# Optimization experiments

Measured on AMD Instinct MI355X. Metric: run time of the kernel, lower is better.

The kernel has to match this reference:

```python
import jax, jax.numpy as jnp
import numpy as np
from jax import lax

H = 1024
NH = 16
R = 32
B, S = 32, 1024
LN_EPS = 1e-5

def _gelu(x):
    return jax.nn.gelu(x, approximate=False)

def setup_inputs() -> dict:
    key = jax.random.key(0)
    ks = jax.random.split(key, 24)
    w = lambda k, shape: jax.random.normal(k, shape, jnp.float32) * 0.02
    d = {}
    d['computation_results'] = jax.random.normal(ks[0], (B, S, H), jnp.float32)
    d['max_steps'] = 16
    # rule selector: Linear(H,H), GELU, Linear(H,R)
    d['rule_w1'] = w(ks[1], (H, H)); d['rule_b1'] = jnp.zeros((H,))
    d['rule_w2'] = w(ks[2], (R, H)); d['rule_b2'] = jnp.zeros((R,))
    d['rule_emb'] = jax.random.normal(ks[3], (R, H), jnp.float32)
    # MultiheadAttention packed in-proj [3H,H] and out-proj [H,H]
    d['attn_in_w'] = w(ks[4], (3 * H, H)); d['attn_in_b'] = jnp.zeros((3 * H,))
    d['attn_out_w'] = w(ks[5], (H, H)); d['attn_out_b'] = jnp.zeros((H,))
    # 2-layer LSTM, PyTorch gate order i,f,g,o
    d['lstm_wih0'] = w(ks[6], (4 * H, H)); d['lstm_whh0'] = w(ks[7], (4 * H, H))
    d['lstm_bih0'] = jnp.zeros((4 * H,)); d['lstm_bhh0'] = jnp.zeros((4 * H,))
    d['lstm_wih1'] = w(ks[8], (4 * H, H)); d['lstm_whh1'] = w(ks[9], (4 * H, H))
    d['lstm_bih1'] = jnp.zeros((4 * H,)); d['lstm_bhh1'] = jnp.zeros((4 * H,))
    # step generator: Linear(H,2H), LayerNorm(2H), GELU, Linear(2H,H)
    d['gen_w1'] = w(ks[10], (2 * H, H)); d['gen_b1'] = jnp.zeros((2 * H,))
    d['gen_ln_g'] = jnp.ones((2 * H,)); d['gen_ln_b'] = jnp.zeros((2 * H,))
    d['gen_w2'] = w(ks[11], (H, 2 * H)); d['gen_b2'] = jnp.zeros((H,))
    # step validator: Linear(2H,H), GELU, Linear(H,1), Sigmoid
    d['val_w1'] = w(ks[12], (H, 2 * H)); d['val_b1'] = jnp.zeros((H,))
    d['val_w2'] = w(ks[13], (1, H)); d['val_b2'] = jnp.zeros((1,))
    # proof verifier: Linear(H,H), GELU, Linear(H,1), Sigmoid
    d['ver_w1'] = w(ks[14], (H, H)); d['ver_b1'] = jnp.zeros((H,))
    d['ver_w2'] = w(ks[15], (1, H)); d['ver_b2'] = jnp.zeros((1,))
    return d


def reference(computation_results, max_steps, rule_w1, rule_b1, rule_w2, rule_b2, rule_emb,
              attn_in_w, attn_in_b, attn_out_w, attn_out_b,
              lstm_wih0, lstm_whh0, lstm_bih0, lstm_bhh0,
              lstm_wih1, lstm_whh1, lstm_bih1, lstm_bhh1,
              gen_w1, gen_b1, gen_ln_g, gen_ln_b, gen_w2, gen_b2,
              val_w1, val_b1, val_w2, val_b2,
              ver_w1, ver_b1, ver_w2, ver_b2):
    comp = computation_results
    b, s, h = comp.shape
    dh = h // NH
    scale = dh ** -0.5
    wq, wk, wv = jnp.split(attn_in_w, 3, axis=0)
    bq, bk, bv = jnp.split(attn_in_b, 3, axis=0)
    # K/V projections of the static context, computed once outside the step loop
    K = (comp @ wk.T + bk).reshape(b, s, NH, dh)  # [B,S,NH,dh]
    V = (comp @ wv.T + bv).reshape(b, s, NH, dh)
    lstm_params = ((lstm_wih0, lstm_whh0, lstm_bih0, lstm_bhh0),
                   (lstm_wih1, lstm_whh1, lstm_bih1, lstm_bhh1))

    def step(carry, _):
        ps, hmem, cmem = carry  # ps: [B,H]; hmem/cmem: [2,B,H]
        # rule selection
        logits = _gelu(ps @ rule_w1.T + rule_b1) @ rule_w2.T + rule_b2
        probs = jax.nn.softmax(logits, axis=-1)  # [B,R]
        sel = probs @ rule_emb  # [B,H]
        # single-query multi-head attention over computation context
        q = (ps @ wq.T + bq).reshape(b, NH, dh) * scale
        scores = jnp.einsum('bhd,bshd->bhs', q, K)
        a = jax.nn.softmax(scores, axis=-1)  # [B,NH,S]
        ctx = jnp.einsum('bhs,bshd->bhd', a, V).reshape(b, h) @ attn_out_w.T + attn_out_b
        attn_avg = a.mean(axis=1)  # head-averaged weights, [B,S]
        # 2-layer LSTM cell, one timestep
        x = ps
        hs, cs = [], []
        for l, (wih, whh, bih, bhh) in enumerate(lstm_params):
            g = x @ wih.T + bih + hmem[l] @ whh.T + bhh
            gi, gf, gg, go = jnp.split(g, 4, axis=-1)
            cn = jax.nn.sigmoid(gf) * cmem[l] + jax.nn.sigmoid(gi) * jnp.tanh(gg)
            hn = jax.nn.sigmoid(go) * jnp.tanh(cn)
            hs.append(hn); cs.append(cn); x = hn
        mem_out = x
        # step generator with LayerNorm+GELU
        si = ps + sel + ctx + mem_out
        z = si @ gen_w1.T + gen_b1
        mu = z.mean(axis=-1, keepdims=True)
        var = ((z - mu) ** 2).mean(axis=-1, keepdims=True)
        z = (z - mu) / jnp.sqrt(var + LN_EPS) * gen_ln_g + gen_ln_b
        nxt = _gelu(z) @ gen_w2.T + gen_b2
        val = jax.nn.sigmoid(_gelu(jnp.concatenate([ps, nxt], axis=-1) @ val_w1.T + val_b1) @ val_w2.T + val_b2)
        return (nxt, jnp.stack(hs), jnp.stack(cs)), (nxt, probs, val, attn_avg)

    init_state = comp[:, 0, :]
    carry0 = (init_state, jnp.zeros((2, b, h), comp.dtype), jnp.zeros((2, b, h), comp.dtype))
    (final, _, _), (steps, probs, vals, attn) = lax.scan(step, carry0, None, length=int(max_steps))
    proof_steps = jnp.concatenate([init_state[None], steps], axis=0)  # [T+1,B,H]
    proof_validity = jax.nn.sigmoid(_gelu(final @ ver_w1.T + ver_b1) @ ver_w2.T + ver_b2)  # [B,1]
    return proof_steps, proof_validity, probs, vals, attn
```

## Files before the change

### kernel.cpp

```cpp
#include <hip/hip_runtime.h>

typedef unsigned short u16;
typedef unsigned int u32;
typedef __attribute__((ext_vector_type(8))) short short8v;
typedef __attribute__((ext_vector_type(4))) float f32x4;

#define MFMA16(a,b,c) __builtin_amdgcn_mfma_f32_16x16x32_bf16((a),(b),(c),0,0,0)

__device__ __forceinline__ u16 f2bf(float f){
  u32 u = __float_as_uint(f);
  return (u16)((u + 0x7fffu + ((u >> 16) & 1u)) >> 16);
}
__device__ __forceinline__ float bf2f(u16 h){ return __uint_as_float(((u32)h) << 16); }
__device__ __forceinline__ float gelu_f(float x){ return 0.5f * x * (1.f + erff(x * 0.70710678118654752f)); }
__device__ __forceinline__ float sigm_f(float x){ return 1.f / (1.f + __expf(-x)); }
__device__ __forceinline__ void acc4(float4& a, const float4 b){ a.x+=b.x; a.y+=b.y; a.z+=b.z; a.w+=b.w; }

__device__ __forceinline__ void gl16(const void* g, void* l){
  __builtin_amdgcn_global_load_lds((const __attribute__((address_space(1))) u32*)g,
                                   (__attribute__((address_space(3))) u32*)l, 16, 0, 0);
}

struct CastJobs { const float* s[13]; u16* d[13]; int start[14]; };
__global__ __launch_bounds__(256) void cast_all_k(CastJobs J){
  int bx = blockIdx.x, j = 0;
  #pragma unroll
  for (int t = 0; t < 13; t++) if (bx >= J.start[t + 1]) j = t + 1;
  int i = (bx - J.start[j]) * 1024 + threadIdx.x * 4;
  float4 v = *(const float4*)(J.s[j] + i);
  ushort4 o; o.x = f2bf(v.x); o.y = f2bf(v.y); o.z = f2bf(v.z); o.w = f2bf(v.w);
  *(ushort4*)(J.d[j] + i) = o;
}

__global__ __launch_bounds__(256) void cast_k(const float* __restrict__ s, u16* __restrict__ d, int n){
  int i = (blockIdx.x * 256 + threadIdx.x) * 4;
  if (i + 3 < n){
    float4 v = *(const float4*)(s + i);
    ushort4 o; o.x = f2bf(v.x); o.y = f2bf(v.y); o.z = f2bf(v.z); o.w = f2bf(v.w);
    *(ushort4*)(d + i) = o;
  }
}

__global__ __launch_bounds__(256) void init_k(const float* __restrict__ comp, float* ps0, float* outp,
                                              float* h0, float* c0, float* h1, float* c1){
  int i = blockIdx.x * 256 + threadIdx.x;
  int b = i >> 10, hh = i & 1023;
  float v = comp[(size_t)b * 1048576 + hh];
  ps0[i] = v; outp[i] = v;
  h0[i] = 0.f; c0[i] = 0.f; h1[i] = 0.f; c1[i] = 0.f;
}

__global__ __launch_bounds__(256) void gemmkv_k(const u16* __restrict__ compb,
    const u16* __restrict__ Wk, const u16* __restrict__ Wv,
    const float* __restrict__ bk, const float* __restrict__ bv,
    u16* __restrict__ Kt, u16* __restrict__ Vb)
{
  __shared__ u16 As[128 * 64];
  __shared__ u16 Bs[128 * 64];
  int tid = threadIdx.x;
  int x = blockIdx.x;
  int xcd = x & 7, p = x >> 3;
  int cpanel = xcd * 32 + (p >> 3);
  int wpanel = p & 7;
  int isK = (blockIdx.z != 0);
  const u16 *msrc, *nsrc; int m0, n0;
  if (!isK){ m0 = cpanel * 128; n0 = wpanel * 128; msrc = compb; nsrc = Wv; }
  else     { m0 = wpanel * 128; n0 = cpanel * 128; msrc = Wk;    nsrc = compb; }

  int w = tid >> 6, l = tid & 63, lr = l & 15, lk = l >> 4;
  int wm = (w >> 1) * 64, wn = (w & 1) * 64;
  f32x4 acc[4][4];
  #pragma unroll
  for (int i = 0; i < 4; i++)
    #pragma unroll
    for (int j = 0; j < 4; j++) acc[i][j] = (f32x4){0.f,0.f,0.f,0.f};

  for (int kc = 0; kc < 1024; kc += 64){
    #pragma unroll
    for (int r = 0; r < 4; r++){
      int s = tid + r * 256;
      int row = s >> 3, pp = s & 7;
      int lg = pp ^ (row & 7);
      gl16(msrc + (size_t)(m0 + row) * 1024 + kc + lg * 8, As + s * 8);
      gl16(nsrc + (size_t)(n0 + row) * 1024 + kc + lg * 8, Bs + s * 8);
    }
    __syncthreads();
    #pragma unroll
    for (int kk = 0; kk < 2; kk++){
      short8v a[4], bb[4];
      #pragma unroll
      for (int mi = 0; mi < 4; mi++){
        int row = wm + mi * 16 + lr;
        int ph = (kk * 4 + lk) ^ (row & 7);
        a[mi] = *(const short8v*)(As + row * 64 + ph * 8);
      }
      #pragma unroll
      for (int ni = 0; ni < 4; ni++){
        int row = wn + ni * 16 + lr;
        int ph = (kk * 4 + lk) ^ (row & 7);
        bb[ni] = *(const short8v*)(Bs + row * 64 + ph * 8);
      }
      #pragma unroll
      for (int mi = 0; mi < 4; mi++)
        #pragma unroll
        for (int ni = 0; ni < 4; ni++)
          acc[mi][ni] = MFMA16(a[mi], bb[ni], acc[mi][ni]);
    }
    __syncthreads();
  }
  #pragma unroll
  for (int mi = 0; mi < 4; mi++)
    #pragma unroll
    for (int ni = 0; ni < 4; ni++)
      #pragma unroll
      for (int r = 0; r < 4; r++){
        int row = m0 + wm + mi * 16 + lk * 4 + r;
        int col = n0 + wn + ni * 16 + lr;
        if (!isK){
          Vb[(size_t)row * 1024 + col] = f2bf(acc[mi][ni][r] + bv[col]);
        } else {
          int b = col >> 10, s = col & 1023;
          Kt[((size_t)b * 1024 + row) * 1024 + s] = f2bf(acc[mi][ni][r] + bk[row]);
        }
      }
}

struct LinSeg {
  const float* X0; const float* Xa; const float* Xb; const float* Xc;
  const u16* W1; const float* b1;
  const float* Y; const u16* W2; const float* b2;
  float* out; float* out2;
  int K1, ld1, K2, ld2, N, act, gate;
  float scale;
  float* stats;
  const float* lng; const float* lnb; const float* lnstats;
  const float* cprev; float* cout; float* hout;
};

__device__ __forceinline__ short8v pack8(float4 v0, float4 v1){
  short8v r;
  r[0]=(short)f2bf(v0.x); r[1]=(short)f2bf(v0.y); r[2]=(short)f2bf(v0.z); r[3]=(short)f2bf(v0.w);
  r[4]=(short)f2bf(v1.x); r[5]=(short)f2bf(v1.y); r[6]=(short)f2bf(v1.z); r[7]=(short)f2bf(v1.w);
  return r;
}

__device__ __forceinline__ short8v load_sum8(const LinSeg& S, int row, int kb){
  size_t o = (size_t)row * S.K1 + kb;
  float4 v0 = *(const float4*)(S.X0 + o);
  float4 v1 = *(const float4*)(S.X0 + o + 4);
  if (S.lng){
    float mu = S.lnstats[row] * (1.f / 2048.f);
    float ms = S.lnstats[32 + row] * (1.f / 2048.f);
    float rstd = rsqrtf(ms - mu * mu + 1e-5f);
    float4 g0 = *(const float4*)(S.lng + kb), g1 = *(const float4*)(S.lng + kb + 4);
    float4 b0 = *(const float4*)(S.lnb + kb), b1 = *(const float4*)(S.lnb + kb + 4);
    v0.x = gelu_f((v0.x - mu) * rstd * g0.x + b0.x);
    v0.y = gelu_f((v0.y - mu) * rstd * g0.y + b0.y);
    v0.z = gelu_f((v0.z - mu) * rstd * g0.z + b0.z);
    v0.w = gelu_f((v0.w - mu) * rstd * g0.w + b0.w);
    v1.x = gelu_f((v1.x - mu) * rstd * g1.x + b1.x);
    v1.y = gelu_f((v1.y - mu) * rstd * g1.y + b1.y);
    v1.z = gelu_f((v1.z - mu) * rstd * g1.z + b1.z);
    v1.w = gelu_f((v1.w - mu) * rstd * g1.w + b1.w);
  } else {
    if (S.Xa){ acc4(v0, *(const float4*)(S.Xa + o)); acc4(v1, *(const float4*)(S.Xa + o + 4)); }
    if (S.Xb){ acc4(v0, *(const float4*)(S.Xb + o)); acc4(v1, *(const float4*)(S.Xb + o + 4)); }
    if (S.Xc){ acc4(v0, *(const float4*)(S.Xc + o)); acc4(v1, *(const float4*)(S.Xc + o + 4)); }
  }
  return pack8(v0, v1);
}
__device__ __forceinline__ short8v load_y8(const float* __restrict__ p){
  return pack8(*(const float4*)(p), *(const float4*)(p + 4));
}

typedef float Red32[32][32];

__device__ void lin_body(const LinSeg& S, int bi, int tid, Red32* red){
  int c0 = bi * 32, j0 = bi * 8;
  int w = tid >> 6, l = tid & 63, lr = l & 15, lk = l >> 4;
  int wc0 = S.gate ? ((lr >> 3) << 10) + j0 + (lr & 7) : c0 + lr;
  int wc1 = S.gate ? (((lr + 16) >> 3) << 10) + j0 + ((lr + 16) & 7) : c0 + lr + 16;
  f32x4 acc[2][2];
  #pragma unroll
  for (int i = 0; i < 2; i++)
    #pragma unroll
    for (int j = 0; j < 2; j++) acc[i][j] = (f32x4){0.f,0.f,0.f,0.f};

  {
    int chunk = S.K1 >> 3;
    int kb0 = w * chunk + lk * 8;
    for (int kk = 0; kk < chunk; kk += 32){
      int kb = kb0 + kk;
      short8v a0 = load_sum8(S, lr, kb);
      short8v a1 = load_sum8(S, lr + 16, kb);
      short8v w0 = *(const short8v*)(S.W1 + (size_t)wc0 * S.ld1 + kb);
      short8v w1 = *(const short8v*)(S.W1 + (size_t)wc1 * S.ld1 + kb);
      acc[0][0] = MFMA16(a0, w0, acc[0][0]);
      acc[0][1] = MFMA16(a0, w1, acc[0][1]);
      acc[1][0] = MFMA16(a1, w0, acc[1][0]);
      acc[1][1] = MFMA16(a1, w1, acc[1][1]);
    }
  }
  if (S.Y){
    int chunk = S.K2 >> 3;
    int kb0 = w * chunk + lk * 8;
    for (int kk = 0; kk < chunk; kk += 32){
      int kb = kb0 + kk;
      short8v a0 = load_y8(S.Y + (size_t)lr * S.K2 + kb);
      short8v a1 = load_y8(S.Y + (size_t)(lr + 16) * S.K2 + kb);
      short8v w0 = *(const short8v*)(S.W2 + (size_t)wc0 * S.ld2 + kb);
      short8v w1 = *(const short8v*)(S.W2 + (size_t)wc1 * S.ld2 + kb);
      acc[0][0] = MFMA16(a0, w0, acc[0][0]);
      acc[0][1] = MFMA16(a0, w1, acc[0][1]);
      acc[1][0] = MFMA16(a1, w0, acc[1][0]);
      acc[1][1] = MFMA16(a1, w1, acc[1][1]);
    }
  }
  #pragma unroll
  for (int mi = 0; mi < 2; mi++)
    #pragma unroll
    for (int ni = 0; ni < 2; ni++)
      #pragma unroll
      for (int r = 0; r < 4; r++)
        red[w][mi * 16 + lk * 4 + r][ni * 16 + lr] = acc[mi][ni][r];
  __syncthreads();
  if (S.gate){
    if (tid < 256){
      int row = tid >> 3, j = tid & 7;
      float s[4];
      #pragma unroll
      for (int g = 0; g < 4; g++){
        float v = 0.f;
        #pragma unroll
        for (int ww = 0; ww < 8; ww++) v += red[ww][row][g * 8 + j];
        s[g] = v;
      }
      int gc = j0 + j;
      float gI = s[0] + S.b1[gc]        + S.b2[gc];
      float gF = s[1] + S.b1[1024 + gc] + S.b2[1024 + gc];
      float gG = s[2] + S.b1[2048 + gc] + S.b2[2048 + gc];
      float gO = s[3] + S.b1[3072 + gc] + S.b2[3072 + gc];
      int idx = row * 1024 + gc;
      float cN = sigm_f(gF) * S.cprev[idx] + sigm_f(gI) * tanhf(gG);
      S.cout[idx] = cN;
      S.hout[idx] = sigm_f(gO) * tanhf(cN);
    }
    return;
  }
  float vout[2]; int iout[2];
  int cnt = 0;
  for (int i = tid; i < 1024; i += 512){
    int row = i >> 5, col = i & 31;
    float v = 0.f;
    #pragma unroll
    for (int ww = 0; ww < 8; ww++) v += red[ww][row][col];
    v += S.b1[c0 + col];
    if (S.b2) v += S.b2[c0 + col];
    if (S.act == 1) v = gelu_f(v);
    else if (S.act == 2) v *= S.scale;
    S.out[(size_t)row * S.N + c0 + col] = v;
    if (S.out2) S.out2[(size_t)row * S.N + c0 + col] = v;
    vout[cnt] = v; iout[cnt] = i; cnt++;
  }
  if (S.stats){
    __syncthreads();
    float* rf = (float*)red;
    rf[iout[0]] = vout[0]; rf[1024 + iout[0]] = vout[0] * vout[0];
    rf[iout[1]] = vout[1]; rf[1024 + iout[1]] = vout[1] * vout[1];
    __syncthreads();
    if (tid < 32){
      float s = 0.f, s2 = 0.f;
      #pragma unroll
      for (int cc = 0; cc < 32; cc++){ s += rf[tid * 32 + cc]; s2 += rf[1024 + tid * 32 + cc]; }
      atomicAdd(S.stats + tid, s);
      atomicAdd(S.stats + 32 + tid, s2);
    }
  }
}

__global__ __launch_bounds__(512) void linmulti_k(LinSeg s0, LinSeg s1, LinSeg s2, int n0, int n1,
                                                  float* zero64){
  __shared__ float red[8][32][32];
  int bx = blockIdx.x, tid = threadIdx.x;
  if (zero64 && bx == 0 && tid < 64) zero64[tid] = 0.f;
  if (bx < n0) lin_body(s0, bx, tid, red);
  else if (bx < n0 + n1) lin_body(s1, bx - n0, tid, red);
  else lin_body(s2, bx - n0 - n1, tid, red);
}

__global__ __launch_bounds__(512) void valver_k(const u16* __restrict__ vw1, const float* __restrict__ vb1,
    const u16* __restrict__ verw1, const float* __restrict__ verb1,
    const float* __restrict__ proof, float* __restrict__ v1){
  __shared__ float red[8][32][32];
  int t = blockIdx.y;
  LinSeg S = {};
  if (t < 16){
    S.X0 = proof + (size_t)t * 32768; S.K1 = 1024; S.W1 = vw1; S.ld1 = 2048; S.b1 = vb1;
    S.Y = proof + (size_t)(t + 1) * 32768; S.K2 = 1024; S.W2 = vw1 + 1024; S.ld2 = 2048;
  } else {
    S.X0 = proof + (size_t)16 * 32768; S.K1 = 1024; S.W1 = verw1; S.ld1 = 1024; S.b1 = verb1;
  }
  S.out = v1 + (size_t)t * 32768; S.N = 1024; S.act = 1;
  lin_body(S, blockIdx.x, threadIdx.x, red);
}

__global__ __launch_bounds__(256) void dotsig_b_k(const float* __restrict__ v1,
    const float* __restrict__ w2v, const float* __restrict__ b2v,
    const float* __restrict__ w2ver, const float* __restrict__ b2ver,
    float* __restrict__ out_vals, float* __restrict__ out_valid){
  int t = blockIdx.x;
  const float* w = (t < 16) ? w2v : w2ver;
  const float* bs = (t < 16) ? b2v : b2ver;
  const float* x = v1 + (size_t)t * 32768;
  int b = threadIdx.x >> 3, l8 = threadIdx.x & 7;
  const float* xr = x + (size_t)b * 1024;
  float acc = 0.f;
  #pragma unroll 8
  for (int kk = 0; kk < 32; kk++){
    int k = kk * 32 + l8 * 4;
    float4 xv = *(const float4*)(xr + k);
    float4 wv = *(const float4*)(w + k);
    acc += xv.x * wv.x + xv.y * wv.y + xv.z * wv.z + xv.w * wv.w;
  }
  acc += __shfl_xor(acc, 1); acc += __shfl_xor(acc, 2); acc += __shfl_xor(acc, 4);
  if (l8 == 0){
    float r = sigm_f(acc + bs[0]);
    if (t < 16) out_vals[t * 32 + b] = r; else out_valid[b] = r;
  }
}

__global__ __launch_bounds__(256) void attn_r2_k(const float* __restrict__ q,
    const u16* __restrict__ Kt, const u16* __restrict__ Vb,
    float* __restrict__ afull, float* __restrict__ ctx0,
    const float* __restrict__ h1a, const float* __restrict__ w2, const float* __restrict__ b2,
    const float* __restrict__ emb, float* __restrict__ probs_out, float* __restrict__ sel)
{
  int tid = threadIdx.x;
  if (blockIdx.x >= 512){
    int b = blockIdx.x - 512;
    __shared__ float lg[32], pshared[32];
    int j = tid >> 3, l8 = tid & 7;
    const float* xr = h1a + b * 1024;
    const float* wr = w2 + j * 1024;
    float acc = 0.f;
    #pragma unroll 8
    for (int kk = 0; kk < 32; kk++){
      int k = kk * 32 + l8 * 4;
      float4 xv = *(const float4*)(xr + k);
      float4 wv = *(const float4*)(wr + k);
      acc += xv.x * wv.x + xv.y * wv.y + xv.z * wv.z + xv.w * wv.w;
    }
    acc += __shfl_xor(acc, 1); acc += __shfl_xor(acc, 2); acc += __shfl_xor(acc, 4);
    if (l8 == 0) lg[j] = acc + b2[j];
    __syncthreads();
    if (tid < 32){
      float v = lg[tid];
      float m = v;
      for (int o = 1; o < 32; o <<= 1) m = fmaxf(m, __shfl_xor(m, o));
      float e = __expf(v - m);
      float s = e;
      for (int o = 1; o < 32; o <<= 1) s += __shfl_xor(s, o);
      float p = e / s;
      pshared[tid] = p;
      probs_out[b * 32 + tid] = p;
    }
    __syncthreads();
    for (int j2 = tid; j2 < 1024; j2 += 256){
      float a2 = 0.f;
      #pragma unroll
      for (int r = 0; r < 32; r++) a2 += pshared[r] * emb[r * 1024 + j2];
      sel[b * 1024 + j2] = a2;
    }
    return;
  }
  int bh = blockIdx.x;
  int b = bh >> 4, h = bh & 15;
  __shared__ float qs[64];
  __shared__ float sc[1024];
  __shared__ float rmx[4], rsm[4];
  __shared__ float ctxp[8][64];
  if (tid < 64) qs[tid] = q[bh * 64 + tid];
  __syncthreads();
  const u32* kt = (const u32*)(Kt + (size_t)bh * 65536);
  float a0 = 0.f, a1 = 0.f, a2 = 0.f, a3 = 0.f;
  #pragma unroll 8
  for (int d = 0; d < 64; d++){
    float qd = qs[d];
    u32 p0 = kt[d * 512 + tid];
    u32 p1 = kt[d * 512 + tid + 256];
    a0 += qd * bf2f((u16)(p0 & 0xffff)); a1 += qd * bf2f((u16)(p0 >> 16));
    a2 += qd * bf2f((u16)(p1 & 0xffff)); a3 += qd * bf2f((u16)(p1 >> 16));
  }
  float mx = fmaxf(fmaxf(a0, a1), fmaxf(a2, a3));
  for (int o = 1; o < 64; o <<= 1) mx = fmaxf(mx, __shfl_xor(mx, o));
  if ((tid & 63) == 0) rmx[tid >> 6] = mx;
  __syncthreads();
  mx = fmaxf(fmaxf(rmx[0], rmx[1]), fmaxf(rmx[2], rmx[3]));
  float e0 = __expf(a0 - mx), e1 = __expf(a1 - mx), e2 = __expf(a2 - mx), e3 = __expf(a3 - mx);
  float sm = e0 + e1 + e2 + e3;
  for (int o = 1; o < 64; o <<= 1) sm += __shfl_xor(sm, o);
  if ((tid & 63) == 0) rsm[tid >> 6] = sm;
  __syncthreads();
  sm = rsm[0] + rsm[1] + rsm[2] + rsm[3];
  float inv = 1.f / sm;
  float* ar = afull + (size_t)bh * 1024;
  float2 w0 = make_float2(e0 * inv, e1 * inv);
  float2 w1 = make_float2(e2 * inv, e3 * inv);
  *(float2*)(sc + 2 * tid) = w0;       *(float2*)(ar + 2 * tid) = w0;
  *(float2*)(sc + 512 + 2 * tid) = w1; *(float2*)(ar + 512 + 2 * tid) = w1;
  __syncthreads();
  int d2 = (tid & 31) * 2, chunk = tid >> 5;
  const u16* vb = Vb + ((size_t)(b * 1024) * 16 + h) * 64 + d2;
  float c0 = 0.f, c1 = 0.f;
  for (int s = chunk * 128; s < chunk * 128 + 128; s++){
    u32 vv = *(const u32*)(vb + (size_t)s * 1024);
    float wv = sc[s];
    c0 += wv * bf2f((u16)(vv & 0xffff));
    c1 += wv * bf2f((u16)(vv >> 16));
  }
  *(float2*)&ctxp[chunk][d2] = make_float2(c0, c1);
  __syncthreads();
  if (tid < 64){
    float r = 0.f;
    #pragma unroll
    for (int c = 0; c < 8; c++) r += ctxp[c][tid];
    ctx0[bh * 64 + tid] = r;
  }
}

__global__ __launch_bounds__(256) void attnavg_all_k(const float* __restrict__ afull, float* __restrict__ out){
  int idx = blockIdx.x * 256 + threadIdx.x;
  int t = idx >> 15, r = idx & 32767;
  int b = r >> 10, s = r & 1023;
  const float* base = afull + (size_t)t * 524288 + (size_t)b * 16384;
  float acc = 0.f;
  #pragma unroll
  for (int h = 0; h < 16; h++) acc += base[h * 1024 + s];
  out[idx] = acc * (1.f / 16.f);
}

extern "C" void kernel_launch(void* const* d_in, const int* in_sizes, int n_in,
                              void* d_out, int out_size, void* d_ws, size_t ws_size,
                              hipStream_t stream) {
  const float* comp      = (const float*)d_in[0];
  const float* rule_w1   = (const float*)d_in[2];
  const float* rule_b1   = (const float*)d_in[3];
  const float* rule_w2   = (const float*)d_in[4];
  const float* rule_b2   = (const float*)d_in[5];
  const float* rule_emb  = (const float*)d_in[6];
  const float* attn_in_w = (const float*)d_in[7];
  const float* attn_in_b = (const float*)d_in[8];
  const float* attn_out_w= (const float*)d_in[9];
  const float* attn_out_b= (const float*)d_in[10];
  const float* wih0 = (const float*)d_in[11];
  const float* whh0 = (const float*)d_in[12];
  const float* bih0 = (const float*)d_in[13];
  const float* bhh0 = (const float*)d_in[14];
  const float* wih1 = (const float*)d_in[15];
  const float* whh1 = (const float*)d_in[16];
  const float* bih1 = (const float*)d_in[17];
  const float* bhh1 = (const float*)d_in[18];
  const float* gen_w1 = (const float*)d_in[19];
  const float* gen_b1 = (const float*)d_in[20];
  const float* ln_g   = (const float*)d_in[21];
  const float* ln_b   = (const float*)d_in[22];
  const float* gen_w2 = (const float*)d_in[23];
  const float* gen_b2 = (const float*)d_in[24];
  const float* val_w1 = (const float*)d_in[25];
  const float* val_b1 = (const float*)d_in[26];
  const float* val_w2 = (const float*)d_in[27];
  const float* val_b2 = (const float*)d_in[28];
  const float* ver_w1 = (const float*)d_in[29];
  const float* ver_b1 = (const float*)d_in[30];
  const float* ver_w2 = (const float*)d_in[31];
  const float* ver_b2 = (const float*)d_in[32];

  float* out_f     = (float*)d_out;
  float* out_proof = out_f;
  float* out_valid = out_f + 17 * 32768;
  float* out_probs = out_valid + 32;
  float* out_vals  = out_probs + 16 * 1024;
  float* out_attn  = out_vals + 16 * 32;

  char* wp = (char*)d_ws;
  auto carve = [&](size_t bytes) -> void* {
    void* p = (void*)wp; wp += (bytes + 255) & ~(size_t)255; return p;
  };
  u16* Kt    = (u16*)carve((size_t)33554432 * 2);
  u16* Vb    = (u16*)carve((size_t)33554432 * 2);
  u16* compb = (u16*)carve((size_t)33554432 * 2);
  float* afull_all = (float*)compb;
  u16* rw1b  = (u16*)carve(2097152);
  u16* wqb   = (u16*)carve(2097152);
  u16* wkb   = (u16*)carve(2097152);
  u16* wvb   = (u16*)carve(2097152);
  u16* aowb  = (u16*)carve(2097152);
  u16* wih0b = (u16*)carve(8388608);
  u16* whh0b = (u16*)carve(8388608);
  u16* wih1b = (u16*)carve(8388608);
  u16* whh1b = (u16*)carve(8388608);
  u16* gw1b  = (u16*)carve(4194304);
  u16* gw2b  = (u16*)carve(4194304);
  u16* vw1b  = (u16*)carve(4194304);
  u16* verw1b= (u16*)carve(2097152);
  float* psb[2]  = { (float*)carve(131072), (float*)carve(131072) };
  float* h0b[2]  = { (float*)carve(131072), (float*)carve(131072) };
  float* c0b[2]  = { (float*)carve(131072), (float*)carve(131072) };
  float* h1b[2]  = { (float*)carve(131072), (float*)carve(131072) };
  float* c1b[2]  = { (float*)carve(131072), (float*)carve(131072) };
  float* h1act = (float*)carve(131072);
  float* sel   = (float*)carve(131072);
  float* qbuf  = (float*)carve(131072);
  float* ctx0  = (float*)carve(131072);
  float* ctxb  = (float*)carve(131072);
  float* zbuf  = (float*)carve(262144);
  float* v1buf = (float*)carve(2228224);
  float* lnstats = (float*)carve(256);
  (void)ws_size; (void)in_sizes; (void)n_in; (void)out_size;

  CastJobs J;
  const float* srcs[13] = { rule_w1, attn_in_w, attn_in_w + 1048576, attn_in_w + 2097152,
                            attn_out_w, wih0, whh0, wih1, whh1, gen_w1, gen_w2, val_w1, ver_w1 };
  u16* dsts[13] = { rw1b, wqb, wkb, wvb, aowb, wih0b, whh0b, wih1b, whh1b, gw1b, gw2b, vw1b, verw1b };
  int sizes[13] = { 1048576, 1048576, 1048576, 1048576, 1048576,
                    4194304, 4194304, 4194304, 4194304, 2097152, 2097152, 2097152, 1048576 };
  int st = 0;
  for (int i = 0; i < 13; i++){ J.s[i] = srcs[i]; J.d[i] = dsts[i]; J.start[i] = st; st += sizes[i] / 1024; }
  J.start[13] = st;
  cast_all_k<<<dim3(st), dim3(256), 0, stream>>>(J);
  cast_k<<<dim3(32768), dim3(256), 0, stream>>>(comp, compb, 33554432);

  gemmkv_k<<<dim3(2048, 1, 2), dim3(256), 0, stream>>>(compb, wkb, wvb,
      attn_in_b + 1024, attn_in_b + 2048, Kt, Vb);

  init_k<<<dim3(128), dim3(256), 0, stream>>>(comp, psb[0], out_proof,
      h0b[0], c0b[0], h1b[0], c1b[0]);

  auto mkseg = [&](const float* X0, const float* Xa, const float* Xb, const float* Xc,
                   int K1, const u16* W1, int ld1, const float* bb1,
                   const float* Y, int K2, const u16* W2, int ld2, const float* bb2,
                   float* out, int N, int act, float scl, float* out2) -> LinSeg {
    LinSeg S = {};
    S.X0 = X0; S.Xa = Xa; S.Xb = Xb; S.Xc = Xc; S.K1 = K1; S.W1 = W1; S.ld1 = ld1; S.b1 = bb1;
    S.Y = Y; S.K2 = K2; S.W2 = W2; S.ld2 = ld2; S.b2 = bb2;
    S.out = out; S.N = N; S.act = act; S.scale = scl; S.out2 = out2;
    return S;
  };
  auto lin1 = [&](LinSeg S){
    linmulti_k<<<dim3(S.N / 32), dim3(512), 0, stream>>>(S, S, S, S.N / 32, 0, nullptr);
  };

  for (int t = 0; t < 16; t++){
    int cur = t & 1, nx = cur ^ 1;
    float* ps = psb[cur];
    float* afull_t = afull_all + (size_t)t * 524288;
    LinSeg sRule = mkseg(ps, 0, 0, 0, 1024, rw1b, 1024, rule_b1, 0, 0, 0, 0, 0, h1act, 1024, 1, 0.f, 0);
    LinSeg sQ    = mkseg(ps, 0, 0, 0, 1024, wqb, 1024, attn_in_b, 0, 0, 0, 0, 0, qbuf, 1024, 2, 0.125f, 0);
    LinSeg sL0   = mkseg(ps, 0, 0, 0, 1024, wih0b, 1024, bih0, h0b[cur], 1024, whh0b, 1024, bhh0,
                         0, 4096, 0, 0.f, 0);
    sL0.gate = 1; sL0.cprev = c0b[cur]; sL0.cout = c0b[nx]; sL0.hout = h0b[nx];
    linmulti_k<<<dim3(192), dim3(512), 0, stream>>>(sRule, sQ, sL0, 32, 32, nullptr);
    attn_r2_k<<<dim3(544), dim3(256), 0, stream>>>(qbuf, Kt, Vb, afull_t, ctx0,
        h1act, rule_w2, rule_b2, rule_emb, out_probs + t * 1024, sel);
    LinSeg sCtx = mkseg(ctx0, 0, 0, 0, 1024, aowb, 1024, attn_out_b, 0, 0, 0, 0, 0, ctxb, 1024, 0, 0.f, 0);
    LinSeg sL1  = mkseg(h0b[nx], 0, 0, 0, 1024, wih1b, 1024, bih1, h1b[cur], 1024, whh1b, 1024, bhh1,
                        0, 4096, 0, 0.f, 0);
    sL1.gate = 1; sL1.cprev = c1b[cur]; sL1.cout = c1b[nx]; sL1.hout = h1b[nx];
    linmulti_k<<<dim3(160), dim3(512), 0, stream>>>(sCtx, sL1, sL1, 32, 128, lnstats);
    LinSeg sG1 = mkseg(ps, sel, ctxb, h1b[nx], 1024, gw1b, 1024, gen_b1, 0, 0, 0, 0, 0,
                       zbuf, 2048, 0, 0.f, 0);
    sG1.stats = lnstats;
    lin1(sG1);
    LinSeg sG2 = mkseg(zbuf, 0, 0, 0, 2048, gw2b, 2048, gen_b2, 0, 0, 0, 0, 0,
                       psb[nx], 1024, 0, 0.f, out_proof + (size_t)(t + 1) * 32768);
    sG2.lng = ln_g; sG2.lnb = ln_b; sG2.lnstats = lnstats;
    lin1(sG2);
  }
  valver_k<<<dim3(32, 17), dim3(512), 0, stream>>>(vw1b, val_b1, verw1b, ver_b1, out_proof, v1buf);
  dotsig_b_k<<<dim3(17), dim3(256), 0, stream>>>(v1buf, val_w2, val_b2, ver_w2, ver_b2,
      out_vals, out_valid);
  attnavg_all_k<<<dim3(2048), dim3(256), 0, stream>>>(afull_all, out_attn);
}
```

Before: 1.925 ms.

## Fuse the 16-step recurrent loop into one persistent kernel with grid barriers

After: 7.126 ms. 3.7x slower.

```diff
diff --git a/kernel.cpp b/kernel.cpp
--- a/kernel.cpp
+++ b/kernel.cpp
@@ -19,6 +19,18 @@
 __device__ __forceinline__ void gl16(const void* g, void* l){
   __builtin_amdgcn_global_load_lds((const __attribute__((address_space(1))) u32*)g,
                                    (__attribute__((address_space(3))) u32*)l, 16, 0, 0);
+}
+
+__device__ __forceinline__ void gbar(unsigned* cnt, unsigned target){
+  __syncthreads();
+  if (threadIdx.x == 0){
+    __threadfence();
+    __hip_atomic_fetch_add(cnt, 1u, __ATOMIC_RELEASE, __HIP_MEMORY_SCOPE_AGENT);
+    while (__hip_atomic_load(cnt, __ATOMIC_ACQUIRE, __HIP_MEMORY_SCOPE_AGENT) < target)
+      __builtin_amdgcn_s_sleep(1);
+    __threadfence();
+  }
+  __syncthreads();
 }
 
 struct CastJobs { const float* s[13]; u16* d[13]; int start[14]; };
@@ -42,7 +54,9 @@
 }
 
 __global__ __launch_bounds__(256) void init_k(const float* __restrict__ comp, float* ps0, float* outp,
-                                              float* h0, float* c0, float* h1, float* c1){
+                                              float* h0, float* c0, float* h1, float* c1,
+                                              unsigned* barcnt){
+  if (blockIdx.x == 0 && threadIdx.x == 0) *barcnt = 0u;
   int i = blockIdx.x * 256 + threadIdx.x;
   int b = i >> 10, hh = i & 1023;
   float v = comp[(size_t)b * 1048576 + hh];
@@ -169,7 +183,7 @@
   }
   return pack8(v0, v1);
 }
-__device__ __forceinline__ short8v load_y8(const float* __restrict__ p){
+__device__ __forceinline__ short8v load_y8(const float* p){
   return pack8(*(const float4*)(p), *(const float4*)(p + 4));
 }
 
@@ -278,14 +292,186 @@
   }
 }
 
-__global__ __launch_bounds__(512) void linmulti_k(LinSeg s0, LinSeg s1, LinSeg s2, int n0, int n1,
-                                                  float* zero64){
+__device__ void attn_job(int bh, int tid, const float* q, const u16* Kt, const u16* Vb,
+                         float* afull, float* ctx0, float* shf){
+  float* qs = shf;
+  float* sc = shf + 64;
+  float* rr = shf + 1088;
+  float* ctxp = shf + 1104;
+  int b = bh >> 4, h = bh & 15;
+  if (tid < 64) qs[tid] = q[bh * 64 + tid];
+  __syncthreads();
+  const u32* kt = (const u32*)(Kt + (size_t)bh * 65536);
+  float a0 = 0.f, a1 = 0.f;
+  #pragma unroll 8
+  for (int d = 0; d < 64; d++){
+    float qd = qs[d];
+    u32 p0 = kt[d * 512 + tid];
+    a0 += qd * bf2f((u16)(p0 & 0xffff));
+    a1 += qd * bf2f((u16)(p0 >> 16));
+  }
+  float mx = fmaxf(a0, a1);
+  for (int o = 1; o < 64; o <<= 1) mx = fmaxf(mx, __shfl_xor(mx, o));
+  if ((tid & 63) == 0) rr[tid >> 6] = mx;
+  __syncthreads();
+  mx = rr[0];
+  #pragma unroll
+  for (int i = 1; i < 8; i++) mx = fmaxf(mx, rr[i]);
+  float e0 = __expf(a0 - mx), e1 = __expf(a1 - mx);
+  float sm = e0 + e1;
+  for (int o = 1; o < 64; o <<= 1) sm += __shfl_xor(sm, o);
+  if ((tid & 63) == 0) rr[8 + (tid >> 6)] = sm;
+  __syncthreads();
+  sm = 0.f;
+  #pragma unroll
+  for (int i = 0; i < 8; i++) sm += rr[8 + i];
+  float inv = 1.f / sm;
+  float2 wv = make_float2(e0 * inv, e1 * inv);
+  *(float2*)(sc + 2 * tid) = wv;
+  *(float2*)(afull + (size_t)bh * 1024 + 2 * tid) = wv;
+  __syncthreads();
+  int d2 = (tid & 31) * 2, chunk = tid >> 5;
+  const u16* vb = Vb + (size_t)(b * 1024 + chunk * 64) * 1024 + h * 64 + d2;
+  const float* scp = sc + chunk * 64;
+  float c0 = 0.f, c1 = 0.f;
+  for (int s = 0; s < 64; s++){
+    u32 vv = *(const u32*)(vb + (size_t)s * 1024);
+    float w = scp[s];
+    c0 += w * bf2f((u16)(vv & 0xffff));
+    c1 += w * bf2f((u16)(vv >> 16));
+  }
+  *(float2*)(ctxp + chunk * 64 + d2) = make_float2(c0, c1);
+  __syncthreads();
+  if (tid < 64){
+    float r = 0.f;
+    #pragma unroll
+    for (int c = 0; c < 16; c++) r += ctxp[c * 64 + tid];
+    ctx0[bh * 64 + tid] = r;
+  }
+}
+
+__device__ void rule2_job(int b, int tid, const float* h1a, const float* w2, const float* b2,
+                          const float* emb, float* probs_out, float* sel, float* shf){
+  float* lg = shf;
+  float* psh = shf + 32;
+  int j = tid >> 4, l16 = tid & 15;
+  const float* xr = h1a + b * 1024;
+  const float* wr = w2 + j * 1024;
+  float acc = 0.f;
+  #pragma unroll 4
+  for (int kk = 0; kk < 16; kk++){
+    int k = kk * 64 + l16 * 4;
+    float4 xv = *(const float4*)(xr + k);
+    float4 wv = *(const float4*)(wr + k);
+    acc += xv.x * wv.x + xv.y * wv.y + xv.z * wv.z + xv.w * wv.w;
+  }
+  acc += __shfl_xor(acc, 1); acc += __shfl_xor(acc, 2);
+  acc += __shfl_xor(acc, 4); acc += __shfl_xor(acc, 8);
+  if (l16 == 0) lg[j] = acc + b2[j];
+  __syncthreads();
+  if (tid < 32){
+    float v = lg[tid];
+    float m = v;
+    for (int o = 1; o < 32; o <<= 1) m = fmaxf(m, __shfl_xor(m, o));
+    float e = __expf(v - m);
+    float s = e;
+    for (int o = 1; o < 32; o <<= 1) s += __shfl_xor(s, o);
+    float p = e / s;
+    psh[tid] = p;
+    probs_out[b * 32 + tid] = p;
+  }
+  __syncthreads();
+  for (int j2 = tid; j2 < 1024; j2 += 512){
+    float a2 = 0.f;
+    #pragma unroll
+    for (int r = 0; r < 32; r++) a2 += psh[r] * emb[r * 1024 + j2];
+    sel[b * 1024 + j2] = a2;
+  }
+}
+
+struct StepParams {
+  const u16 *rw1b, *wqb, *wih0b, *whh0b, *aowb, *wih1b, *whh1b, *gw1b, *gw2b;
+  const float *rule_b1, *attn_in_b, *bih0, *bhh0, *rule_w2, *rule_b2, *rule_emb;
+  const float *attn_out_b, *bih1, *bhh1, *gen_b1, *gen_b2, *ln_g, *ln_b;
+  const u16 *Kt, *Vb;
+  float *ps0, *ps1, *h0a, *h0bb, *c0a, *c0bb, *h1aa, *h1bb, *c1a, *c1bb;
+  float *h1act, *sel, *qbuf, *ctx0, *ctxb, *zbuf, *lnstats;
+  float *afull_all, *out_probs, *out_proof;
+  unsigned* barcnt;
+};
+
+__global__ __launch_bounds__(512) void steploop_k(StepParams P){
   __shared__ float red[8][32][32];
+  float* shf = &red[0][0][0];
   int bx = blockIdx.x, tid = threadIdx.x;
-  if (zero64 && bx == 0 && tid < 64) zero64[tid] = 0.f;
-  if (bx < n0) lin_body(s0, bx, tid, red);
-  else if (bx < n0 + n1) lin_body(s1, bx - n0, tid, red);
-  else lin_body(s2, bx - n0 - n1, tid, red);
+  unsigned tgt = 0;
+  for (int t = 0; t < 16; t++){
+    float *ps, *psn, *h0c, *h0n, *c0c, *c0n, *h1c, *h1n, *c1c, *c1n;
+    if ((t & 1) == 0){
+      ps = P.ps0;  psn = P.ps1;
+      h0c = P.h0a; h0n = P.h0bb; c0c = P.c0a; c0n = P.c0bb;
+      h1c = P.h1aa; h1n = P.h1bb; c1c = P.c1a; c1n = P.c1bb;
+    } else {
+      ps = P.ps1;  psn = P.ps0;
+      h0c = P.h0bb; h0n = P.h0a; c0c = P.c0bb; c0n = P.c0a;
+      h1c = P.h1bb; h1n = P.h1aa; c1c = P.c1bb; c1n = P.c1a;
+    }
+    float* afull_t = P.afull_all + (size_t)t * 524288;
+
+    if (bx < 32){
+      LinSeg S = {}; S.X0 = ps; S.K1 = 1024; S.W1 = P.rw1b; S.ld1 = 1024; S.b1 = P.rule_b1;
+      S.out = P.h1act; S.N = 1024; S.act = 1;
+      lin_body(S, bx, tid, red);
+    } else if (bx < 64){
+      LinSeg S = {}; S.X0 = ps; S.K1 = 1024; S.W1 = P.wqb; S.ld1 = 1024; S.b1 = P.attn_in_b;
+      S.out = P.qbuf; S.N = 1024; S.act = 2; S.scale = 0.125f;
+      lin_body(S, bx - 32, tid, red);
+    } else if (bx < 192){
+      LinSeg S = {}; S.X0 = ps; S.K1 = 1024; S.W1 = P.wih0b; S.ld1 = 1024; S.b1 = P.bih0;
+      S.Y = h0c; S.K2 = 1024; S.W2 = P.whh0b; S.ld2 = 1024; S.b2 = P.bhh0;
+      S.gate = 1; S.cprev = c0c; S.cout = c0n; S.hout = h0n;
+      lin_body(S, bx - 64, tid, red);
+    }
+    gbar(P.barcnt, tgt += 256);
+
+    for (int j = bx; j < 544; j += 256){
+      if (j < 512) attn_job(j, tid, P.qbuf, P.Kt, P.Vb, afull_t, P.ctx0, shf);
+      else rule2_job(j - 512, tid, P.h1act, P.rule_w2, P.rule_b2, P.rule_emb,
+                     P.out_probs + t * 1024, P.sel, shf);
+      __syncthreads();
+    }
+    gbar(P.barcnt, tgt += 256);
+
+    if (bx < 32){
+      LinSeg S = {}; S.X0 = P.ctx0; S.K1 = 1024; S.W1 = P.aowb; S.ld1 = 1024; S.b1 = P.attn_out_b;
+      S.out = P.ctxb; S.N = 1024;
+      lin_body(S, bx, tid, red);
+    } else if (bx < 160){
+      LinSeg S = {}; S.X0 = h0n; S.K1 = 1024; S.W1 = P.wih1b; S.ld1 = 1024; S.b1 = P.bih1;
+      S.Y = h1c; S.K2 = 1024; S.W2 = P.whh1b; S.ld2 = 1024; S.b2 = P.bhh1;
+      S.gate = 1; S.cprev = c1c; S.cout = c1n; S.hout = h1n;
+      lin_body(S, bx - 32, tid, red);
+    } else if (bx == 255 && tid < 64){
+      P.lnstats[tid] = 0.f;
+    }
+    gbar(P.barcnt, tgt += 256);
+
+    if (bx < 64){
+      LinSeg S = {}; S.X0 = ps; S.Xa = P.sel; S.Xb = P.ctxb; S.Xc = h1n;
+      S.K1 = 1024; S.W1 = P.gw1b; S.ld1 = 1024; S.b1 = P.gen_b1;
+      S.out = P.zbuf; S.N = 2048; S.stats = P.lnstats;
+      lin_body(S, bx, tid, red);
+    }
+    gbar(P.barcnt, tgt += 256);
+
+    if (bx < 32){
+      LinSeg S = {}; S.X0 = P.zbuf; S.K1 = 2048; S.W1 = P.gw2b; S.ld1 = 2048; S.b1 = P.gen_b2;
+      S.out = psn; S.N = 1024; S.out2 = P.out_proof + (size_t)(t + 1) * 32768;
+      S.lng = P.ln_g; S.lnb = P.ln_b; S.lnstats = P.lnstats;
+      lin_body(S, bx, tid, red);
+    }
+    gbar(P.barcnt, tgt += 256);
+  }
 }
 
 __global__ __launch_bounds__(512) void valver_k(const u16* __restrict__ vw1, const float* __restrict__ vb1,
@@ -326,105 +512,6 @@
   if (l8 == 0){
     float r = sigm_f(acc + bs[0]);
     if (t < 16) out_vals[t * 32 + b] = r; else out_valid[b] = r;
-  }
-}
-
-__global__ __launch_bounds__(256) void attn_r2_k(const float* __restrict__ q,
-    const u16* __restrict__ Kt, const u16* __restrict__ Vb,
-    float* __restrict__ afull, float* __restrict__ ctx0,
-    const float* __restrict__ h1a, const float* __restrict__ w2, const float* __restrict__ b2,
-    const float* __restrict__ emb, float* __restrict__ probs_out, float* __restrict__ sel)
-{
-  int tid = threadIdx.x;
-  if (blockIdx.x >= 512){
-    int b = blockIdx.x - 512;
-    __shared__ float lg[32], pshared[32];
-    int j = tid >> 3, l8 = tid & 7;
-    const float* xr = h1a + b * 1024;
-    const float* wr = w2 + j * 1024;
-    float acc = 0.f;
-    #pragma unroll 8
-    for (int kk = 0; kk < 32; kk++){
-      int k = kk * 32 + l8 * 4;
-      float4 xv = *(const float4*)(xr + k);
-      float4 wv = *(const float4*)(wr + k);
-      acc += xv.x * wv.x + xv.y * wv.y + xv.z * wv.z + xv.w * wv.w;
-    }
-    acc += __shfl_xor(acc, 1); acc += __shfl_xor(acc, 2); acc += __shfl_xor(acc, 4);
-    if (l8 == 0) lg[j] = acc + b2[j];
-    __syncthreads();
-    if (tid < 32){
-      float v = lg[tid];
-      float m = v;
-      for (int o = 1; o < 32; o <<= 1) m = fmaxf(m, __shfl_xor(m, o));
-      float e = __expf(v - m);
-      float s = e;
-      for (int o = 1; o < 32; o <<= 1) s += __shfl_xor(s, o);
-      float p = e / s;
-      pshared[tid] = p;
-      probs_out[b * 32 + tid] = p;
-    }
-    __syncthreads();
-    for (int j2 = tid; j2 < 1024; j2 += 256){
-      float a2 = 0.f;
-      #pragma unroll
-      for (int r = 0; r < 32; r++) a2 += pshared[r] * emb[r * 1024 + j2];
-      sel[b * 1024 + j2] = a2;
-    }
-    return;
-  }
-  int bh = blockIdx.x;
-  int b = bh >> 4, h = bh & 15;
-  __shared__ float qs[64];
-  __shared__ float sc[1024];
-  __shared__ float rmx[4], rsm[4];
-  __shared__ float ctxp[8][64];
-  if (tid < 64) qs[tid] = q[bh * 64 + tid];
-  __syncthreads();
-  const u32* kt = (const u32*)(Kt + (size_t)bh * 65536);
-  float a0 = 0.f, a1 = 0.f, a2 = 0.f, a3 = 0.f;
-  #pragma unroll 8
-  for (int d = 0; d < 64; d++){
-    float qd = qs[d];
-    u32 p0 = kt[d * 512 + tid];
-    u32 p1 = kt[d * 512 + tid + 256];
-    a0 += qd * bf2f((u16)(p0 & 0xffff)); a1 += qd * bf2f((u16)(p0 >> 16));
-    a2 += qd * bf2f((u16)(p1 & 0xffff)); a3 += qd * bf2f((u16)(p1 >> 16));
-  }
-  float mx = fmaxf(fmaxf(a0, a1), fmaxf(a2, a3));
-  for (int o = 1; o < 64; o <<= 1) mx = fmaxf(mx, __shfl_xor(mx, o));
-  if ((tid & 63) == 0) rmx[tid >> 6] = mx;
-  __syncthreads();
-  mx = fmaxf(fmaxf(rmx[0], rmx[1]), fmaxf(rmx[2], rmx[3]));
-  float e0 = __expf(a0 - mx), e1 = __expf(a1 - mx), e2 = __expf(a2 - mx), e3 = __expf(a3 - mx);
-  float sm = e0 + e1 + e2 + e3;
-  for (int o = 1; o < 64; o <<= 1) sm += __shfl_xor(sm, o);
-  if ((tid & 63) == 0) rsm[tid >> 6] = sm;
-  __syncthreads();
-  sm = rsm[0] + rsm[1] + rsm[2] + rsm[3];
-  float inv = 1.f / sm;
-  float* ar = afull + (size_t)bh * 1024;
-  float2 w0 = make_float2(e0 * inv, e1 * inv);
-  float2 w1 = make_float2(e2 * inv, e3 * inv);
-  *(float2*)(sc + 2 * tid) = w0;       *(float2*)(ar + 2 * tid) = w0;
-  *(float2*)(sc + 512 + 2 * tid) = w1; *(float2*)(ar + 512 + 2 * tid) = w1;
-  __syncthreads();
-  int d2 = (tid & 31) * 2, chunk = tid >> 5;
-  const u16* vb = Vb + ((size_t)(b * 1024) * 16 + h) * 64 + d2;
-  float c0 = 0.f, c1 = 0.f;
-  for (int s = chunk * 128; s < chunk * 128 + 128; s++){
-    u32 vv = *(const u32*)(vb + (size_t)s * 1024);
-    float wv = sc[s];
-    c0 += wv * bf2f((u16)(vv & 0xffff));
-    c1 += wv * bf2f((u16)(vv >> 16));
-  }
-  *(float2*)&ctxp[chunk][d2] = make_float2(c0, c1);
-  __syncthreads();
-  if (tid < 64){
-    float r = 0.f;
-    #pragma unroll
-    for (int c = 0; c < 8; c++) r += ctxp[c][tid];
-    ctx0[bh * 64 + tid] = r;
   }
 }
 
@@ -516,6 +603,7 @@
   float* zbuf  = (float*)carve(262144);
   float* v1buf = (float*)carve(2228224);
   float* lnstats = (float*)carve(256);
+  unsigned* barcnt = (unsigned*)carve(256);
   (void)ws_size; (void)in_sizes; (void)n_in; (void)out_size;
 
   CastJobs J;
@@ -534,48 +622,25 @@
       attn_in_b + 1024, attn_in_b + 2048, Kt, Vb);
 
   init_k<<<dim3(128), dim3(256), 0, stream>>>(comp, psb[0], out_proof,
-      h0b[0], c0b[0], h1b[0], c1b[0]);
-
-  auto mkseg = [&](const float* X0, const float* Xa, const float* Xb, const float* Xc,
-                   int K1, const u16* W1, int ld1, const float* bb1,
-                   const float* Y, int K2, const u16* W2, int ld2, const float* bb2,
-                   float* out, int N, int act, float scl, float* out2) -> LinSeg {
-    LinSeg S = {};
-    S.X0 = X0; S.Xa = Xa; S.Xb = Xb; S.Xc = Xc; S.K1 = K1; S.W1 = W1; S.ld1 = ld1; S.b1 = bb1;
-    S.Y = Y; S.K2 = K2; S.W2 = W2; S.ld2 = ld2; S.b2 = bb2;
-    S.out = out; S.N = N; S.act = act; S.scale = scl; S.out2 = out2;
-    return S;
-  };
-  auto lin1 = [&](LinSeg S){
-    linmulti_k<<<dim3(S.N / 32), dim3(512), 0, stream>>>(S, S, S, S.N / 32, 0, nullptr);
-  };
-
-  for (int t = 0; t < 16; t++){
-    int cur = t & 1, nx = cur ^ 1;
-    float* ps = psb[cur];
-    float* afull_t = afull_all + (size_t)t * 524288;
-    LinSeg sRule = mkseg(ps, 0, 0, 0, 1024, rw1b, 1024, rule_b1, 0, 0, 0, 0, 0, h1act, 1024, 1, 0.f, 0);
-    LinSeg sQ    = mkseg(ps, 0, 0, 0, 1024, wqb, 1024, attn_in_b, 0, 0, 0, 0, 0, qbuf, 1024, 2, 0.125f, 0);
-    LinSeg sL0   = mkseg(ps, 0, 0, 0, 1024, wih0b, 1024, bih0, h0b[cur], 1024, whh0b, 1024, bhh0,
-                         0, 4096, 0, 0.f, 0);
-    sL0.gate = 1; sL0.cprev = c0b[cur]; sL0.cout = c0b[nx]; sL0.hout = h0b[nx];
-    linmulti_k<<<dim3(192), dim3(512), 0, stream>>>(sRule, sQ, sL0, 32, 32, nullptr);
-    attn_r2_k<<<dim3(544), dim3(256), 0, stream>>>(qbuf, Kt, Vb, afull_t, ctx0,
-        h1act, rule_w2, rule_b2, rule_emb, out_probs + t * 1024, sel);
-    LinSeg sCtx = mkseg(ctx0, 0, 0, 0, 1024, aowb, 1024, attn_out_b, 0, 0, 0, 0, 0, ctxb, 1024, 0, 0.f, 0);
-    LinSeg sL1  = mkseg(h0b[nx], 0, 0, 0, 1024, wih1b, 1024, bih1, h1b[cur], 1024, whh1b, 1024, bhh1,
-                        0, 4096, 0, 0.f, 0);
-    sL1.gate = 1; sL1.cprev = c1b[cur]; sL1.cout = c1b[nx]; sL1.hout = h1b[nx];
-    linmulti_k<<<dim3(160), dim3(512), 0, stream>>>(sCtx, sL1, sL1, 32, 128, lnstats);
-    LinSeg sG1 = mkseg(ps, sel, ctxb, h1b[nx], 1024, gw1b, 1024, gen_b1, 0, 0, 0, 0, 0,
-                       zbuf, 2048, 0, 0.f, 0);
-    sG1.stats = lnstats;
-    lin1(sG1);
-    LinSeg sG2 = mkseg(zbuf, 0, 0, 0, 2048, gw2b, 2048, gen_b2, 0, 0, 0, 0, 0,
-                       psb[nx], 1024, 0, 0.f, out_proof + (size_t)(t + 1) * 32768);
-    sG2.lng = ln_g; sG2.lnb = ln_b; sG2.lnstats = lnstats;
-    lin1(sG2);
-  }
+      h0b[0], c0b[0], h1b[0], c1b[0], barcnt);
+
+  StepParams P;
+  P.rw1b = rw1b; P.wqb = wqb; P.wih0b = wih0b; P.whh0b = whh0b; P.aowb = aowb;
+  P.wih1b = wih1b; P.whh1b = whh1b; P.gw1b = gw1b; P.gw2b = gw2b;
+  P.rule_b1 = rule_b1; P.attn_in_b = attn_in_b; P.bih0 = bih0; P.bhh0 = bhh0;
+  P.rule_w2 = rule_w2; P.rule_b2 = rule_b2; P.rule_emb = rule_emb;
+  P.attn_out_b = attn_out_b; P.bih1 = bih1; P.bhh1 = bhh1;
+  P.gen_b1 = gen_b1; P.gen_b2 = gen_b2; P.ln_g = ln_g; P.ln_b = ln_b;
+  P.Kt = Kt; P.Vb = Vb;
+  P.ps0 = psb[0]; P.ps1 = psb[1];
+  P.h0a = h0b[0]; P.h0bb = h0b[1]; P.c0a = c0b[0]; P.c0bb = c0b[1];
+  P.h1aa = h1b[0]; P.h1bb = h1b[1]; P.c1a = c1b[0]; P.c1bb = c1b[1];
+  P.h1act = h1act; P.sel = sel; P.qbuf = qbuf; P.ctx0 = ctx0; P.ctxb = ctxb;
+  P.zbuf = zbuf; P.lnstats = lnstats;
+  P.afull_all = afull_all; P.out_probs = out_probs; P.out_proof = out_proof;
+  P.barcnt = barcnt;
+  steploop_k<<<dim3(256), dim3(512), 0, stream>>>(P);
+
   valver_k<<<dim3(32, 17), dim3(512), 0, stream>>>(vw1b, val_b1, verw1b, ver_b1, out_proof, v1buf);
   dotsig_b_k<<<dim3(17), dim3(256), 0, stream>>>(v1buf, val_w2, val_b2, ver_w2, ver_b2,
       out_vals, out_valid);
```
